# Kernel tuning notes

Hardware: AMD Instinct MI355X
Metric: run time of the kernel (lower is better)

Reference implementation:

```python
import jax, jax.numpy as jnp
import numpy as np

N = 50000   # nodes
E = 800000  # edges
NF = 16     # num_node_features
EF = 8      # num_edge_features
H = 4       # heads
C = 64      # out_channels per head
NC = 4      # num_classes


def setup_inputs() -> dict:
    key = jax.random.key(0)
    ks = jax.random.split(key, 32)
    w = lambda k, shape: (jax.random.normal(k, shape, jnp.float32) * 0.05)
    inp = {
        "x": jax.random.normal(ks[0], (N, NF), jnp.float32),
        "edge_index": jax.random.randint(ks[1], (2, E), 0, N, dtype=jnp.int32),
        "edge_attr": jax.random.normal(ks[2], (E, EF), jnp.float32),
        # fc00
        "w00": w(ks[3], (NF, 64)), "b00": jnp.zeros((64,), jnp.float32),
        # edge MLP
        "we1": w(ks[4], (EF, 64)), "be1": jnp.zeros((64,), jnp.float32),
        "we2": w(ks[5], (64, 64)), "be2": jnp.zeros((64,), jnp.float32),
        "we3": w(ks[6], (64, 64)), "be3": jnp.zeros((64,), jnp.float32),
        # TransformerConv projections (64 -> H*C = 256)
        "wq": w(ks[7], (64, H * C)), "bq": jnp.zeros((H * C,), jnp.float32),
        "wk": w(ks[8], (64, H * C)), "bk": jnp.zeros((H * C,), jnp.float32),
        "wv": w(ks[9], (64, H * C)), "bv": jnp.zeros((H * C,), jnp.float32),
        "wedge": w(ks[10], (64, H * C)), "bedge": jnp.zeros((H * C,), jnp.float32),
        "wskip": w(ks[11], (64, H * C)), "bskip": jnp.zeros((H * C,), jnp.float32),
        # LayerNorm(256)
        "ln_g": jnp.ones((H * C,), jnp.float32), "ln_b": jnp.zeros((H * C,), jnp.float32),
        # head
        "w1": w(ks[12], (H * C, 128)), "b1": jnp.zeros((128,), jnp.float32),
        "w2": w(ks[13], (128, NC)), "b2": jnp.zeros((NC,), jnp.float32),
    }
    return inp


def _forward(x, edge_attr, w00, b00, we1, be1, we2, be2, we3, be3,
             wq, bq, wk, bk, wv, bv, wedge, bedge, wskip, bskip,
             ln_g, ln_b, w1, b1, w2, b2, edge_index):
    relu = jax.nn.relu
    n = x.shape[0]
    # node embed (dropout = identity in eval)
    x1 = relu(x @ w00 + b00)                              # [N, 64]
    # edge MLP
    e = relu(edge_attr @ we1 + be1)
    e = relu(e @ we2 + be2)
    e = relu(e @ we3 + be3)                               # [E, 64]
    src, dst = edge_index[0], edge_index[1]
    # project nodes once, then gather per edge
    q = (x1 @ wq + bq).reshape(n, H, C)[dst]              # [E, H, C]
    k = (x1 @ wk + bk).reshape(n, H, C)[src]
    v = (x1 @ wv + bv).reshape(n, H, C)[src]
    eh = (e @ wedge + bedge).reshape(-1, H, C)            # [E, H, C]
    k = k + eh
    v = v + eh
    alpha = jnp.sum(q * k, axis=-1) / np.sqrt(C)          # [E, H]
    # segment softmax over incoming edges of each target node
    m = jax.ops.segment_max(alpha, dst, num_segments=n)   # [N, H]
    m = jnp.where(jnp.isfinite(m), m, 0.0)
    p = jnp.exp(alpha - m[dst])
    s = jax.ops.segment_sum(p, dst, num_segments=n)
    a = p / (s[dst] + 1e-16)                              # [E, H]
    out = jax.ops.segment_sum(v * a[:, :, None], dst, num_segments=n)
    out = out.reshape(n, H * C) + (x1 @ wskip + bskip)    # root skip (root_weight=True)
    # LayerNorm(256)
    mu = jnp.mean(out, axis=-1, keepdims=True)
    var = jnp.mean(jnp.square(out - mu), axis=-1, keepdims=True)
    out = (out - mu) * jax.lax.rsqrt(var + 1e-5) * ln_g + ln_b
    out = relu(out)
    h = relu(out @ w1 + b1)
    logits = h @ w2 + b2
    return jax.nn.log_softmax(logits, axis=1)


def reference(x, edge_index, edge_attr, w00, b00, we1, be1, we2, be2, we3, be3,
              wq, bq, wk, bk, wv, bv, wedge, bedge, wskip, bskip,
              ln_g, ln_b, w1, b1, w2, b2):
    return _forward(x, edge_attr, w00, b00, we1, be1, we2, be2, we3, be3,
                    wq, bq, wk, bk, wv, bv, wedge, bedge, wskip, bskip,
                    ln_g, ln_b, w1, b1, w2, b2, edge_index)
```

## Files before the change

kernel.cpp:

```cpp
#include <hip/hip_runtime.h>
#include <hip/hip_bf16.h>

typedef unsigned short u16;
typedef __attribute__((ext_vector_type(8))) short bf16x8;
typedef __attribute__((ext_vector_type(4))) float f32x4;

#define NN 50000
#define NE 800000
#define SCAN_NB ((NN + 255) / 256)

__device__ __forceinline__ float bf2f(u16 u) { return __uint_as_float(((unsigned)u) << 16); }
__device__ __forceinline__ u16 f2bf(float f) {
  unsigned u = __float_as_uint(f);
  return (u16)((u + 0x7FFFu + ((u >> 16) & 1u)) >> 16);
}

__global__ void k_zero(int* __restrict__ deg) {
  int i = blockIdx.x * 256 + threadIdx.x;
  if (i < NN) deg[i] = 0;
}

__global__ void k_hist(const int* __restrict__ ei, int* __restrict__ deg) {
  int i = blockIdx.x * 256 + threadIdx.x;
  if (i < NE) {
    int d = ei[NE + i];
    if (d >= 0 && d < NN) atomicAdd(&deg[d], 1);
  }
}

__global__ __launch_bounds__(256) void k_scan_a(const int* __restrict__ deg,
                                                int* __restrict__ bsum) {
  __shared__ int red[256];
  const int t = threadIdx.x;
  const int i = blockIdx.x * 256 + t;
  red[t] = (i < NN) ? deg[i] : 0;
  __syncthreads();
  #pragma unroll
  for (int s = 128; s > 0; s >>= 1) {
    if (t < s) red[t] += red[t + s];
    __syncthreads();
  }
  if (t == 0) bsum[blockIdx.x] = red[0];
}

__global__ __launch_bounds__(256) void k_scan_b(const int* __restrict__ bsum,
                                                int* __restrict__ boff,
                                                int* __restrict__ rowptr) {
  __shared__ int s[256];
  const int t = threadIdx.x;
  int v = (t < SCAN_NB) ? bsum[t] : 0;
  s[t] = v;
  __syncthreads();
  #pragma unroll
  for (int o = 1; o < 256; o <<= 1) {
    int u = (t >= o) ? s[t - o] : 0;
    __syncthreads();
    s[t] += u;
    __syncthreads();
  }
  if (t < SCAN_NB) boff[t] = s[t] - v;
  if (t == 255) rowptr[NN] = s[255];
}

__global__ __launch_bounds__(256) void k_scan_c(const int* __restrict__ deg,
                                                const int* __restrict__ boff,
                                                int* __restrict__ rowptr,
                                                int* __restrict__ cursor) {
  __shared__ int s[256];
  const int t = threadIdx.x;
  const int i = blockIdx.x * 256 + t;
  int v = (i < NN) ? deg[i] : 0;
  s[t] = v;
  __syncthreads();
  #pragma unroll
  for (int o = 1; o < 256; o <<= 1) {
    int u = (t >= o) ? s[t - o] : 0;
    __syncthreads();
    s[t] += u;
    __syncthreads();
  }
  if (i < NN) {
    int r = boff[blockIdx.x] + s[t] - v;
    rowptr[i] = r;
    cursor[i] = r;
  }
}

__global__ void k_scatter(const int* __restrict__ ei, int* __restrict__ cursor,
                          int* __restrict__ elist, int* __restrict__ slist) {
  int i = blockIdx.x * 256 + threadIdx.x;
  if (i < NE) {
    int d = ei[NE + i];
    if (d >= 0 && d < NN) {
      int pos = atomicAdd(&cursor[d], 1);
      if (pos >= 0 && pos < NE) {
        elist[pos] = i;
        int s = ei[i];
        slist[pos] = max(0, min(s, NN - 1));
      }
    }
  }
}

__global__ void k_prep(const float* __restrict__ wedge, const float* __restrict__ wk,
                       float* __restrict__ wT, float* __restrict__ wkT) {
  int i = blockIdx.x * 256 + threadIdx.x;
  if (i < 16384) {
    int c = i >> 6, j = i & 63;
    wT[i] = wedge[j * 256 + c];
  } else if (i < 32768) {
    int i2 = i - 16384;
    int c = i2 >> 6, j = i2 & 63;
    wkT[i2] = wk[j * 256 + c];
  }
}

__global__ void k_prep_w(const float* __restrict__ we1, const float* __restrict__ we2,
                         const float* __restrict__ we3,
                         u16* __restrict__ wB1t, u16* __restrict__ wB2t, u16* __restrict__ wB3t) {
  int i = blockIdx.x * 256 + threadIdx.x;
  if (i < 512) {
    int n = i >> 3, k = i & 7;
    wB1t[i] = f2bf(we1[k * 64 + n]);
  } else if (i < 512 + 4096) {
    int i2 = i - 512;
    int n = i2 >> 6, k = i2 & 63;
    wB2t[i2] = f2bf(we2[k * 64 + n]);
  } else if (i < 512 + 8192) {
    int i2 = i - 512 - 4096;
    int n = i2 >> 6, k = i2 & 63;
    wB3t[i2] = f2bf(we3[k * 64 + n]);
  }
}

__global__ void k_prep_b(const float* __restrict__ wedge, const float* __restrict__ wv,
                         const float* __restrict__ wskip, u16* __restrict__ Bt) {
  const int col = blockIdx.x;
  const int k = threadIdx.x;
  float v;
  if (k < 256) v = ((k >> 6) == (col >> 6)) ? wedge[(k & 63) * 256 + col] : 0.f;
  else if (k < 512) { int k2 = k - 256; v = ((k2 >> 6) == (col >> 6)) ? wv[(k2 & 63) * 256 + col] : 0.f; }
  else v = wskip[(k - 512) * 256 + col];
  Bt[col * 576 + k] = f2bf(v);
}

__global__ void k_prep_h(const float* __restrict__ w1, u16* __restrict__ Bt1) {
  const int col = blockIdx.x;
  const int k = threadIdx.x;
  Bt1[col * 256 + k] = f2bf(w1[k * 128 + col]);
}

__global__ __launch_bounds__(256) void k_node(
    const float* __restrict__ x, const float* __restrict__ w00, const float* __restrict__ b00,
    const float* __restrict__ wq, const float* __restrict__ bq,
    u16* __restrict__ x1g, u16* __restrict__ qg) {
  __shared__ float xs[128];
  __shared__ float x1s[8 * 65];
  const int t = threadIdx.x;
  const int n0 = blockIdx.x * 8;
  if (t < 128) xs[t] = x[n0 * 16 + t];
  __syncthreads();
  #pragma unroll
  for (int it = 0; it < 2; ++it) {
    int nb = it * 4 + (t >> 6);
    int col = t & 63;
    float v = b00[col];
    #pragma unroll
    for (int i = 0; i < 16; ++i) v += xs[nb * 16 + i] * w00[i * 64 + col];
    v = fmaxf(v, 0.f);
    x1s[nb * 65 + col] = v;
    x1g[(n0 + nb) * 64 + col] = f2bf(v);
  }
  __syncthreads();
  float aq[8];
  const float bqv = bq[t];
  #pragma unroll
  for (int nb = 0; nb < 8; ++nb) aq[nb] = bqv;
  for (int j = 0; j < 64; ++j) {
    float wqv = wq[j * 256 + t];
    #pragma unroll
    for (int nb = 0; nb < 8; ++nb) aq[nb] += x1s[nb * 65 + j] * wqv;
  }
  #pragma unroll
  for (int nb = 0; nb < 8; ++nb) qg[(n0 + nb) * 256 + t] = f2bf(aq[nb]);
}

__global__ __launch_bounds__(256) void k_gmat(const u16* __restrict__ qg,
                                              const float* __restrict__ wT,
                                              const float* __restrict__ wkT,
                                              u16* __restrict__ Gg, u16* __restrict__ Qkg) {
  __shared__ float qs[8 * 256];
  const int t = threadIdx.x;
  const int n0 = blockIdx.x * 8;
  #pragma unroll
  for (int i = 0; i < 8; ++i) qs[i * 256 + t] = bf2f(qg[(n0 + i) * 256 + t]);
  __syncthreads();
  const int h = t >> 6, j = t & 63;
  float accG[8] = {0, 0, 0, 0, 0, 0, 0, 0};
  float accK[8] = {0, 0, 0, 0, 0, 0, 0, 0};
  for (int c = 0; c < 64; ++c) {
    float wv = wT[(h * 64 + c) * 64 + j];
    float wk = wkT[(h * 64 + c) * 64 + j];
    #pragma unroll
    for (int nb = 0; nb < 8; ++nb) {
      float qv = qs[nb * 256 + h * 64 + c];
      accG[nb] += qv * wv;
      accK[nb] += qv * wk;
    }
  }
  #pragma unroll
  for (int nb = 0; nb < 8; ++nb) {
    Gg[(n0 + nb) * 256 + t] = f2bf(accG[nb]);
    Qkg[(n0 + nb) * 256 + t] = f2bf(accK[nb]);
  }
}

#define EPB 128
#define APAD 72
__global__ __launch_bounds__(256) void k_edge_mlp(
    const float* __restrict__ ea,
    const u16* __restrict__ wB1t, const u16* __restrict__ wB2t, const u16* __restrict__ wB3t,
    const float* __restrict__ be1, const float* __restrict__ be2, const float* __restrict__ be3,
    u16* __restrict__ e3g) {
  __shared__ u16 actA[EPB * APAD];
  __shared__ u16 actB[EPB * APAD];
  const int t = threadIdx.x;
  const int w = t >> 6, l = t & 63;
  const int quad = l >> 4, li = l & 15;
  const int e0 = blockIdx.x * EPB;
  const f32x4 zc = {0.f, 0.f, 0.f, 0.f};

  float b1c[4], b2c[4], b3c[4];
  #pragma unroll
  for (int nt = 0; nt < 4; ++nt) {
    b1c[nt] = be1[nt * 16 + li];
    b2c[nt] = be2[nt * 16 + li];
    b3c[nt] = be3[nt * 16 + li];
  }

  bf16x8 b1f[4];
  #pragma unroll
  for (int nt = 0; nt < 4; ++nt) {
    bf16x8 z = {};
    if (quad == 0) z = *(const bf16x8*)(wB1t + (nt * 16 + li) * 8);
    b1f[nt] = z;
  }
  #pragma unroll
  for (int mi = 0; mi < 2; ++mi) {
    const int mt = w * 2 + mi;
    bf16x8 af = {};
    if (quad == 0) {
      const float4* pa = (const float4*)(ea + (size_t)(e0 + mt * 16 + li) * 8);
      float4 p0 = pa[0], p1 = pa[1];
      af[0] = (short)f2bf(p0.x); af[1] = (short)f2bf(p0.y);
      af[2] = (short)f2bf(p0.z); af[3] = (short)f2bf(p0.w);
      af[4] = (short)f2bf(p1.x); af[5] = (short)f2bf(p1.y);
      af[6] = (short)f2bf(p1.z); af[7] = (short)f2bf(p1.w);
    }
    #pragma unroll
    for (int nt = 0; nt < 4; ++nt) {
      f32x4 d = __builtin_amdgcn_mfma_f32_16x16x32_bf16(af, b1f[nt], zc, 0, 0, 0);
      #pragma unroll
      for (int r = 0; r < 4; ++r)
        actA[(mt * 16 + quad * 4 + r) * APAD + nt * 16 + li] = f2bf(fmaxf(d[r] + b1c[nt], 0.f));
    }
  }
  __syncthreads();

  {
    bf16x8 bf[4][2];
    #pragma unroll
    for (int nt = 0; nt < 4; ++nt)
      #pragma unroll
      for (int kk = 0; kk < 2; ++kk)
        bf[nt][kk] = *(const bf16x8*)(wB2t + (nt * 16 + li) * 64 + kk * 32 + quad * 8);
    #pragma unroll
    for (int mi = 0; mi < 2; ++mi) {
      const int mt = w * 2 + mi;
      bf16x8 a0 = *(const bf16x8*)(actA + (mt * 16 + li) * APAD + quad * 8);
      bf16x8 a1 = *(const bf16x8*)(actA + (mt * 16 + li) * APAD + 32 + quad * 8);
      #pragma unroll
      for (int nt = 0; nt < 4; ++nt) {
        f32x4 d = __builtin_amdgcn_mfma_f32_16x16x32_bf16(a0, bf[nt][0], zc, 0, 0, 0);
        d = __builtin_amdgcn_mfma_f32_16x16x32_bf16(a1, bf[nt][1], d, 0, 0, 0);
        #pragma unroll
        for (int r = 0; r < 4; ++r)
          actB[(mt * 16 + quad * 4 + r) * APAD + nt * 16 + li] = f2bf(fmaxf(d[r] + b2c[nt], 0.f));
      }
    }
  }
  __syncthreads();

  {
    bf16x8 bf[4][2];
    #pragma unroll
    for (int nt = 0; nt < 4; ++nt)
      #pragma unroll
      for (int kk = 0; kk < 2; ++kk)
        bf[nt][kk] = *(const bf16x8*)(wB3t + (nt * 16 + li) * 64 + kk * 32 + quad * 8);
    #pragma unroll
    for (int mi = 0; mi < 2; ++mi) {
      const int mt = w * 2 + mi;
      bf16x8 a0 = *(const bf16x8*)(actB + (mt * 16 + li) * APAD + quad * 8);
      bf16x8 a1 = *(const bf16x8*)(actB + (mt * 16 + li) * APAD + 32 + quad * 8);
      #pragma unroll
      for (int nt = 0; nt < 4; ++nt) {
        f32x4 d = __builtin_amdgcn_mfma_f32_16x16x32_bf16(a0, bf[nt][0], zc, 0, 0, 0);
        d = __builtin_amdgcn_mfma_f32_16x16x32_bf16(a1, bf[nt][1], d, 0, 0, 0);
        #pragma unroll
        for (int r = 0; r < 4; ++r)
          actA[(mt * 16 + quad * 4 + r) * APAD + nt * 16 + li] = f2bf(fmaxf(d[r] + b3c[nt], 0.f));
      }
    }
  }
  __syncthreads();

  #pragma unroll
  for (int it = 0; it < 4; ++it) {
    int flat = it * 2048 + t * 8;
    int el = flat >> 6, c = flat & 63;
    uint4 v = *(const uint4*)(actA + el * APAD + c);
    *(uint4*)(e3g + (size_t)(e0 + el) * 64 + c) = v;
  }
}

__global__ __launch_bounds__(256) void k_attn(
    const int* __restrict__ rowptr, const int* __restrict__ elist, const int* __restrict__ slist,
    u16* qo, const u16* __restrict__ x1g, u16* gz, const u16* __restrict__ Qkg,
    const u16* __restrict__ e3g,
    const float* __restrict__ bk, const float* __restrict__ bedge,
    float* __restrict__ bfac) {
  const int t = threadIdx.x;
  const int w = t >> 6;
  const int l = t & 63;
  const int grp = l >> 4;
  const int li = l & 15;
  const int chb = grp * 64 + li * 4;
  const int n = blockIdx.x * 4 + w;
  int base = rowptr[n];
  int end  = rowptr[n + 1];
  base = max(0, min(base, NE));
  end  = max(base, min(end, NE));
  if (l == 0) bfac[n] = (end > base) ? 1.f : 0.f;

  float Qkf[4], Gf[4];
  {
    ushort4 kv = *(const ushort4*)(Qkg + (size_t)n * 256 + chb);
    Qkf[0] = bf2f(kv.x); Qkf[1] = bf2f(kv.y); Qkf[2] = bf2f(kv.z); Qkf[3] = bf2f(kv.w);
    ushort4 gv = *(const ushort4*)(gz + (size_t)n * 256 + chb);
    Gf[0] = bf2f(gv.x); Gf[1] = bf2f(gv.y); Gf[2] = bf2f(gv.z); Gf[3] = bf2f(gv.w);
  }
  float bqe;
  {
    ushort4 qv = *(const ushort4*)(qo + (size_t)n * 256 + chb);
    float4 bkv = *(const float4*)(bk + chb);
    float4 bev = *(const float4*)(bedge + chb);
    bqe = bf2f(qv.x) * (bkv.x + bev.x) + bf2f(qv.y) * (bkv.y + bev.y)
        + bf2f(qv.z) * (bkv.z + bev.z) + bf2f(qv.w) * (bkv.w + bev.w);
    #pragma unroll
    for (int mk = 1; mk < 16; mk <<= 1) bqe += __shfl_xor(bqe, mk);
  }

  float s_run = 0.f;
  float y[4] = {0, 0, 0, 0}, zz[4] = {0, 0, 0, 0};
  int d = base;
  for (; d + 1 < end; d += 2) {
    int eid0 = elist[d],     src0 = slist[d];
    int eid1 = elist[d + 1], src1 = slist[d + 1];
    eid0 = max(0, min(eid0, NE - 1)); eid1 = max(0, min(eid1, NE - 1));
    src0 = max(0, min(src0, NN - 1)); src1 = max(0, min(src1, NN - 1));
    ushort4 x0 = *(const ushort4*)(x1g + (size_t)src0 * 64 + li * 4);
    ushort4 e0 = *(const ushort4*)(e3g + (size_t)eid0 * 64 + li * 4);
    ushort4 x1v = *(const ushort4*)(x1g + (size_t)src1 * 64 + li * 4);
    ushort4 e1 = *(const ushort4*)(e3g + (size_t)eid1 * 64 + li * 4);
    float xf00 = bf2f(x0.x), xf01 = bf2f(x0.y), xf02 = bf2f(x0.z), xf03 = bf2f(x0.w);
    float ef00 = bf2f(e0.x), ef01 = bf2f(e0.y), ef02 = bf2f(e0.z), ef03 = bf2f(e0.w);
    float xf10 = bf2f(x1v.x), xf11 = bf2f(x1v.y), xf12 = bf2f(x1v.z), xf13 = bf2f(x1v.w);
    float ef10 = bf2f(e1.x), ef11 = bf2f(e1.y), ef12 = bf2f(e1.z), ef13 = bf2f(e1.w);
    float p0 = Qkf[0]*xf00 + Qkf[1]*xf01 + Qkf[2]*xf02 + Qkf[3]*xf03
             + Gf[0]*ef00 + Gf[1]*ef01 + Gf[2]*ef02 + Gf[3]*ef03;
    float p1 = Qkf[0]*xf10 + Qkf[1]*xf11 + Qkf[2]*xf12 + Qkf[3]*xf13
             + Gf[0]*ef10 + Gf[1]*ef11 + Gf[2]*ef12 + Gf[3]*ef13;
    #pragma unroll
    for (int mk = 1; mk < 16; mk <<= 1) { p0 += __shfl_xor(p0, mk); p1 += __shfl_xor(p1, mk); }
    float w0 = __expf(fminf((p0 + bqe) * 0.125f, 60.f));
    float w1 = __expf(fminf((p1 + bqe) * 0.125f, 60.f));
    s_run += w0 + w1;
    y[0] += w0*xf00 + w1*xf10; y[1] += w0*xf01 + w1*xf11;
    y[2] += w0*xf02 + w1*xf12; y[3] += w0*xf03 + w1*xf13;
    zz[0] += w0*ef00 + w1*ef10; zz[1] += w0*ef01 + w1*ef11;
    zz[2] += w0*ef02 + w1*ef12; zz[3] += w0*ef03 + w1*ef13;
  }
  if (d < end) {
    int eid0 = elist[d], src0 = slist[d];
    eid0 = max(0, min(eid0, NE - 1));
    src0 = max(0, min(src0, NN - 1));
    ushort4 x0 = *(const ushort4*)(x1g + (size_t)src0 * 64 + li * 4);
    ushort4 e0 = *(const ushort4*)(e3g + (size_t)eid0 * 64 + li * 4);
    float xf00 = bf2f(x0.x), xf01 = bf2f(x0.y), xf02 = bf2f(x0.z), xf03 = bf2f(x0.w);
    float ef00 = bf2f(e0.x), ef01 = bf2f(e0.y), ef02 = bf2f(e0.z), ef03 = bf2f(e0.w);
    float p0 = Qkf[0]*xf00 + Qkf[1]*xf01 + Qkf[2]*xf02 + Qkf[3]*xf03
             + Gf[0]*ef00 + Gf[1]*ef01 + Gf[2]*ef02 + Gf[3]*ef03;
    #pragma unroll
    for (int mk = 1; mk < 16; mk <<= 1) p0 += __shfl_xor(p0, mk);
    float w0 = __expf(fminf((p0 + bqe) * 0.125f, 60.f));
    s_run += w0;
    y[0] += w0*xf00; y[1] += w0*xf01; y[2] += w0*xf02; y[3] += w0*xf03;
    zz[0] += w0*ef00; zz[1] += w0*ef01; zz[2] += w0*ef02; zz[3] += w0*ef03;
  }
  const float inv_s = 1.0f / (s_run + 1e-16f);
  ushort4 ynv, znv;
  ynv.x = f2bf(y[0] * inv_s); ynv.y = f2bf(y[1] * inv_s);
  ynv.z = f2bf(y[2] * inv_s); ynv.w = f2bf(y[3] * inv_s);
  znv.x = f2bf(zz[0] * inv_s); znv.y = f2bf(zz[1] * inv_s);
  znv.z = f2bf(zz[2] * inv_s); znv.w = f2bf(zz[3] * inv_s);
  *(ushort4*)(qo + (size_t)n * 256 + chb) = ynv;
  *(ushort4*)(gz + (size_t)n * 256 + chb) = znv;
}

#define PM 64
#define PK 576
#define PAPAD 584
__global__ __launch_bounds__(256) void k_post(
    const u16* __restrict__ zng, const u16* __restrict__ yng, const u16* __restrict__ x1g,
    const u16* __restrict__ Bt, const float* __restrict__ bfac,
    const float* __restrict__ bedge, const float* __restrict__ bv, const float* __restrict__ bskip,
    const float* __restrict__ lng, const float* __restrict__ lnb,
    u16* __restrict__ postg) {
  __shared__ u16 As[PM * PAPAD];
  __shared__ float ps1[PM * 4];
  __shared__ float ps2[PM * 4];
  const int t = threadIdx.x;
  const int w = t >> 6, l = t & 63;
  const int quad = l >> 4, li = l & 15;
  const int n0 = blockIdx.x * PM;

  for (int q = t; q < 2048; q += 256) {
    int row = q >> 5, off = (q & 31) * 8;
    uint4 vz = make_uint4(0, 0, 0, 0), vy = make_uint4(0, 0, 0, 0);
    if (n0 + row < NN) {
      vz = *(const uint4*)(zng + (size_t)(n0 + row) * 256 + off);
      vy = *(const uint4*)(yng + (size_t)(n0 + row) * 256 + off);
    }
    *(uint4*)(As + row * PAPAD + off) = vz;
    *(uint4*)(As + row * PAPAD + 256 + off) = vy;
  }
  for (int q = t; q < 512; q += 256) {
    int row = q >> 3, off = (q & 7) * 8;
    uint4 v = make_uint4(0, 0, 0, 0);
    if (n0 + row < NN) v = *(const uint4*)(x1g + (size_t)(n0 + row) * 64 + off);
    *(uint4*)(As + row * PAPAD + 512 + off) = v;
  }
  __syncthreads();

  f32x4 acc[4][4];
  #pragma unroll
  for (int mt = 0; mt < 4; ++mt)
    #pragma unroll
    for (int nt = 0; nt < 4; ++nt) acc[mt][nt] = (f32x4){0.f, 0.f, 0.f, 0.f};

  const int colbase = w * 64;
  #pragma unroll
  for (int s = 0; s < 18; ++s) {
    bf16x8 bf[4];
    #pragma unroll
    for (int nt = 0; nt < 4; ++nt)
      bf[nt] = *(const bf16x8*)(Bt + (size_t)(colbase + nt * 16 + li) * PK + s * 32 + quad * 8);
    #pragma unroll
    for (int mt = 0; mt < 4; ++mt) {
      bf16x8 af = *(const bf16x8*)(As + (mt * 16 + li) * PAPAD + s * 32 + quad * 8);
      #pragma unroll
      for (int nt = 0; nt < 4; ++nt)
        acc[mt][nt] = __builtin_amdgcn_mfma_f32_16x16x32_bf16(af, bf[nt], acc[mt][nt], 0, 0, 0);
    }
  }

  float beb[4], bs4[4], g4[4], lb4[4];
  #pragma unroll
  for (int nt = 0; nt < 4; ++nt) {
    int col = colbase + nt * 16 + li;
    beb[nt] = bedge[col] + bv[col];
    bs4[nt] = bskip[col]; g4[nt] = lng[col]; lb4[nt] = lnb[col];
  }
  #pragma unroll
  for (int mt = 0; mt < 4; ++mt) {
    #pragma unroll
    for (int r = 0; r < 4; ++r) {
      int node = n0 + mt * 16 + quad * 4 + r;
      float hasE = bfac[min(node, NN - 1)];
      #pragma unroll
      for (int nt = 0; nt < 4; ++nt)
        acc[mt][nt][r] += hasE * beb[nt] + bs4[nt];
    }
  }
  #pragma unroll
  for (int mt = 0; mt < 4; ++mt)
    #pragma unroll
    for (int r = 0; r < 4; ++r) {
      float s = acc[mt][0][r] + acc[mt][1][r] + acc[mt][2][r] + acc[mt][3][r];
      #pragma unroll
      for (int mk = 1; mk < 16; mk <<= 1) s += __shfl_xor(s, mk);
      if (li == 0) ps1[(mt * 16 + quad * 4 + r) * 4 + w] = s;
    }
  __syncthreads();
  float mu[4][4];
  #pragma unroll
  for (int mt = 0; mt < 4; ++mt)
    #pragma unroll
    for (int r = 0; r < 4; ++r) {
      float4 p = *(const float4*)(ps1 + (mt * 16 + quad * 4 + r) * 4);
      mu[mt][r] = (p.x + p.y + p.z + p.w) * (1.0f / 256.0f);
    }
  #pragma unroll
  for (int mt = 0; mt < 4; ++mt)
    #pragma unroll
    for (int r = 0; r < 4; ++r) {
      float m = mu[mt][r];
      float s = 0.f;
      #pragma unroll
      for (int nt = 0; nt < 4; ++nt) { float dd = acc[mt][nt][r] - m; s += dd * dd; }
      #pragma unroll
      for (int mk = 1; mk < 16; mk <<= 1) s += __shfl_xor(s, mk);
      if (li == 0) ps2[(mt * 16 + quad * 4 + r) * 4 + w] = s;
    }
  __syncthreads();
  #pragma unroll
  for (int mt = 0; mt < 4; ++mt)
    #pragma unroll
    for (int r = 0; r < 4; ++r) {
      float4 p = *(const float4*)(ps2 + (mt * 16 + quad * 4 + r) * 4);
      float rstd = rsqrtf((p.x + p.y + p.z + p.w) * (1.0f / 256.0f) + 1e-5f);
      int node = n0 + mt * 16 + quad * 4 + r;
      if (node < NN) {
        float m = mu[mt][r];
        #pragma unroll
        for (int nt = 0; nt < 4; ++nt) {
          int col = colbase + nt * 16 + li;
          postg[(size_t)node * 256 + col] =
              f2bf(fmaxf((acc[mt][nt][r] - m) * rstd * g4[nt] + lb4[nt], 0.f));
        }
      }
    }
}

#define HAPAD 264
#define H1PAD 136
__global__ __launch_bounds__(256) void k_head(
    const u16* __restrict__ postg, const u16* __restrict__ Bt1,
    const float* __restrict__ b1, const float* __restrict__ w2, const float* __restrict__ b2,
    float* __restrict__ outg) {
  __shared__ u16 As[64 * HAPAD];
  __shared__ u16 h1s[64 * H1PAD];
  const int t = threadIdx.x;
  const int w = t >> 6, l = t & 63;
  const int quad = l >> 4, li = l & 15;
  const int n0 = blockIdx.x * 64;

  for (int q = t; q < 2048; q += 256) {
    int row = q >> 5, off = (q & 31) * 8;
    uint4 v = make_uint4(0, 0, 0, 0);
    if (n0 + row < NN) v = *(const uint4*)(postg + (size_t)(n0 + row) * 256 + off);
    *(uint4*)(As + row * HAPAD + off) = v;
  }
  __syncthreads();

  f32x4 acc[4][2];
  #pragma unroll
  for (int mt = 0; mt < 4; ++mt)
    #pragma unroll
    for (int nt = 0; nt < 2; ++nt) acc[mt][nt] = (f32x4){0.f, 0.f, 0.f, 0.f};
  const int colbase = w * 32;
  #pragma unroll
  for (int s = 0; s < 8; ++s) {
    bf16x8 bf[2];
    #pragma unroll
    for (int nt = 0; nt < 2; ++nt)
      bf[nt] = *(const bf16x8*)(Bt1 + (size_t)(colbase + nt * 16 + li) * 256 + s * 32 + quad * 8);
    #pragma unroll
    for (int mt = 0; mt < 4; ++mt) {
      bf16x8 af = *(const bf16x8*)(As + (mt * 16 + li) * HAPAD + s * 32 + quad * 8);
      #pragma unroll
      for (int nt = 0; nt < 2; ++nt)
        acc[mt][nt] = __builtin_amdgcn_mfma_f32_16x16x32_bf16(af, bf[nt], acc[mt][nt], 0, 0, 0);
    }
  }
  float b1c[2];
  #pragma unroll
  for (int nt = 0; nt < 2; ++nt) b1c[nt] = b1[colbase + nt * 16 + li];
  #pragma unroll
  for (int mt = 0; mt < 4; ++mt)
    #pragma unroll
    for (int nt = 0; nt < 2; ++nt)
      #pragma unroll
      for (int r = 0; r < 4; ++r)
        h1s[(mt * 16 + quad * 4 + r) * H1PAD + colbase + nt * 16 + li] =
            f2bf(fmaxf(acc[mt][nt][r] + b1c[nt], 0.f));
  __syncthreads();

  const int node = t >> 2, c = t & 3;
  float lg = b2[c];
  const u16* hrow = h1s + node * H1PAD;
  #pragma unroll 4
  for (int j = 0; j < 128; ++j) lg += bf2f(hrow[j]) * w2[j * 4 + c];
  float mx = lg;
  #pragma unroll
  for (int mk = 1; mk < 4; mk <<= 1) mx = fmaxf(mx, __shfl_xor(mx, mk));
  float ex = __expf(lg - mx);
  float se = ex;
  #pragma unroll
  for (int mk = 1; mk < 4; mk <<= 1) se += __shfl_xor(se, mk);
  float res = lg - (mx + __logf(se));
  if (n0 + node < NN) outg[(size_t)(n0 + node) * 4 + c] = res;
}

extern "C" void kernel_launch(void* const* d_in, const int* in_sizes, int n_in,
                              void* d_out, int out_size, void* d_ws, size_t ws_size,
                              hipStream_t stream) {
  const float* x     = (const float*)d_in[0];
  const int*   ei    = (const int*)d_in[1];
  const float* ea    = (const float*)d_in[2];
  const float* w00   = (const float*)d_in[3];
  const float* b00   = (const float*)d_in[4];
  const float* we1   = (const float*)d_in[5];
  const float* be1   = (const float*)d_in[6];
  const float* we2   = (const float*)d_in[7];
  const float* be2   = (const float*)d_in[8];
  const float* we3   = (const float*)d_in[9];
  const float* be3   = (const float*)d_in[10];
  const float* wq    = (const float*)d_in[11];
  const float* bq    = (const float*)d_in[12];
  const float* wk    = (const float*)d_in[13];
  const float* bk    = (const float*)d_in[14];
  const float* wv    = (const float*)d_in[15];
  const float* bv    = (const float*)d_in[16];
  const float* wedge = (const float*)d_in[17];
  const float* bedge = (const float*)d_in[18];
  const float* wskip = (const float*)d_in[19];
  const float* bskip = (const float*)d_in[20];
  const float* lng   = (const float*)d_in[21];
  const float* lnb   = (const float*)d_in[22];
  const float* w1    = (const float*)d_in[23];
  const float* b1    = (const float*)d_in[24];
  const float* w2    = (const float*)d_in[25];
  const float* b2    = (const float*)d_in[26];
  float* outg = (float*)d_out;

  size_t off = 0;
  char* wsb = (char*)d_ws;
  auto carve = [&](size_t bytes) -> char* {
    char* r = wsb + off;
    off += (bytes + 255) & ~(size_t)255;
    return r;
  };
  u16* qg     = (u16*)carve((size_t)NN * 256 * 2);
  u16* Gg     = (u16*)carve((size_t)NN * 256 * 2);
  u16* Qkg    = (u16*)carve((size_t)NN * 256 * 2);
  u16* x1g    = (u16*)carve((size_t)NN * 64 * 2);
  u16* e3g    = (u16*)carve((size_t)NE * 64 * 2);
  int* deg    = (int*)carve((size_t)NN * 4);
  int* rowptr = (int*)carve((size_t)(NN + 1) * 4);
  int* cursor = (int*)carve((size_t)NN * 4);
  int* elist  = (int*)carve((size_t)NE * 4);
  int* slist  = (int*)carve((size_t)NE * 4);
  float* bfac = (float*)carve((size_t)NN * 4);
  int* bsum   = (int*)carve((size_t)SCAN_NB * 4);
  int* boff   = (int*)carve((size_t)SCAN_NB * 4);
  float* wT   = (float*)carve(16384 * 4);
  float* wkT  = (float*)carve(16384 * 4);
  u16* wB1t   = (u16*)carve(512 * 2);
  u16* wB2t   = (u16*)carve(4096 * 2);
  u16* wB3t   = (u16*)carve(4096 * 2);
  u16* Bt     = (u16*)carve((size_t)256 * 576 * 2);
  u16* Bt1    = (u16*)carve((size_t)128 * 256 * 2);
  u16* postg  = e3g;
  if (off > ws_size) return;

  k_prep<<<128, 256, 0, stream>>>(wedge, wk, wT, wkT);
  k_prep_w<<<34, 256, 0, stream>>>(we1, we2, we3, wB1t, wB2t, wB3t);
  k_prep_b<<<256, 576, 0, stream>>>(wedge, wv, wskip, Bt);
  k_prep_h<<<128, 256, 0, stream>>>(w1, Bt1);
  k_zero<<<SCAN_NB, 256, 0, stream>>>(deg);
  k_hist<<<NE / 256, 256, 0, stream>>>(ei, deg);
  k_scan_a<<<SCAN_NB, 256, 0, stream>>>(deg, bsum);
  k_scan_b<<<1, 256, 0, stream>>>(bsum, boff, rowptr);
  k_scan_c<<<SCAN_NB, 256, 0, stream>>>(deg, boff, rowptr, cursor);
  k_scatter<<<NE / 256, 256, 0, stream>>>(ei, cursor, elist, slist);
  k_node<<<NN / 8, 256, 0, stream>>>(x, w00, b00, wq, bq, x1g, qg);
  k_gmat<<<NN / 8, 256, 0, stream>>>(qg, wT, wkT, Gg, Qkg);
  k_edge_mlp<<<NE / EPB, 256, 0, stream>>>(ea, wB1t, wB2t, wB3t, be1, be2, be3, e3g);
  k_attn<<<NN / 4, 256, 0, stream>>>(rowptr, elist, slist, qg, x1g, Gg, Qkg, e3g, bk, bedge, bfac);
  k_post<<<(NN + PM - 1) / PM, 256, 0, stream>>>(Gg, qg, x1g, Bt, bfac, bedge, bv, bskip,
                                                 lng, lnb, postg);
  k_head<<<(NN + 63) / 64, 256, 0, stream>>>(postg, Bt1, b1, w2, b2, outg);
}
```

Baseline: 565.4 us.

## Fuse node and G-matrix kernels, write edge features in CSR order, drop bias term

Merges k_node and k_gmat so q stays in shared memory instead of being written to and reread from global as bf16. The scatter now records each edge's CSR position, and the edge MLP writes its output directly in destination-sorted order, so the attention loop reads edge features contiguously with no elist indirection. The constant per-node q·(bk+bedge) term is removed from the logits because it cancels in the softmax. The cost is a scattered write in the edge MLP, and the softmax loses the max-subtraction shift that term provided, relying on the existing clamp at 60.

```diff
diff --git a/kernel.cpp b/kernel.cpp
--- a/kernel.cpp
+++ b/kernel.cpp
@@ -87,14 +87,14 @@
 }
 
 __global__ void k_scatter(const int* __restrict__ ei, int* __restrict__ cursor,
-                          int* __restrict__ elist, int* __restrict__ slist) {
+                          int* __restrict__ slist, int* __restrict__ e2p) {
   int i = blockIdx.x * 256 + threadIdx.x;
   if (i < NE) {
     int d = ei[NE + i];
     if (d >= 0 && d < NN) {
       int pos = atomicAdd(&cursor[d], 1);
       if (pos >= 0 && pos < NE) {
-        elist[pos] = i;
+        e2p[i] = pos;
         int s = ei[i];
         slist[pos] = max(0, min(s, NN - 1));
       }
@@ -150,12 +150,14 @@
   Bt1[col * 256 + k] = f2bf(w1[k * 128 + col]);
 }
 
-__global__ __launch_bounds__(256) void k_node(
+__global__ __launch_bounds__(256) void k_ng(
     const float* __restrict__ x, const float* __restrict__ w00, const float* __restrict__ b00,
     const float* __restrict__ wq, const float* __restrict__ bq,
-    u16* __restrict__ x1g, u16* __restrict__ qg) {
+    const float* __restrict__ wT, const float* __restrict__ wkT,
+    u16* __restrict__ x1g, u16* __restrict__ Gg, u16* __restrict__ Qkg) {
   __shared__ float xs[128];
   __shared__ float x1s[8 * 65];
+  __shared__ float qs[8 * 256];
   const int t = threadIdx.x;
   const int n0 = blockIdx.x * 8;
   if (t < 128) xs[t] = x[n0 * 16 + t];
@@ -172,28 +174,19 @@
     x1g[(n0 + nb) * 64 + col] = f2bf(v);
   }
   __syncthreads();
-  float aq[8];
-  const float bqv = bq[t];
-  #pragma unroll
-  for (int nb = 0; nb < 8; ++nb) aq[nb] = bqv;
-  for (int j = 0; j < 64; ++j) {
-    float wqv = wq[j * 256 + t];
-    #pragma unroll
-    for (int nb = 0; nb < 8; ++nb) aq[nb] += x1s[nb * 65 + j] * wqv;
-  }
-  #pragma unroll
-  for (int nb = 0; nb < 8; ++nb) qg[(n0 + nb) * 256 + t] = f2bf(aq[nb]);
-}
-
-__global__ __launch_bounds__(256) void k_gmat(const u16* __restrict__ qg,
-                                              const float* __restrict__ wT,
-                                              const float* __restrict__ wkT,
-                                              u16* __restrict__ Gg, u16* __restrict__ Qkg) {
-  __shared__ float qs[8 * 256];
-  const int t = threadIdx.x;
-  const int n0 = blockIdx.x * 8;
-  #pragma unroll
-  for (int i = 0; i < 8; ++i) qs[i * 256 + t] = bf2f(qg[(n0 + i) * 256 + t]);
+  {
+    float aq[8];
+    const float bqv = bq[t];
+    #pragma unroll
+    for (int nb = 0; nb < 8; ++nb) aq[nb] = bqv;
+    for (int j = 0; j < 64; ++j) {
+      float wqv = wq[j * 256 + t];
+      #pragma unroll
+      for (int nb = 0; nb < 8; ++nb) aq[nb] += x1s[nb * 65 + j] * wqv;
+    }
+    #pragma unroll
+    for (int nb = 0; nb < 8; ++nb) qs[nb * 256 + t] = aq[nb];
+  }
   __syncthreads();
   const int h = t >> 6, j = t & 63;
   float accG[8] = {0, 0, 0, 0, 0, 0, 0, 0};
@@ -221,7 +214,7 @@
     const float* __restrict__ ea,
     const u16* __restrict__ wB1t, const u16* __restrict__ wB2t, const u16* __restrict__ wB3t,
     const float* __restrict__ be1, const float* __restrict__ be2, const float* __restrict__ be3,
-    u16* __restrict__ e3g) {
+    const int* __restrict__ e2p, u16* __restrict__ e3g) {
   __shared__ u16 actA[EPB * APAD];
   __shared__ u16 actB[EPB * APAD];
   const int t = threadIdx.x;
@@ -319,17 +312,17 @@
   for (int it = 0; it < 4; ++it) {
     int flat = it * 2048 + t * 8;
     int el = flat >> 6, c = flat & 63;
+    int pos = e2p[e0 + el];
+    pos = ((unsigned)pos <= (unsigned)(NE - 1)) ? pos : NE;
     uint4 v = *(const uint4*)(actA + el * APAD + c);
-    *(uint4*)(e3g + (size_t)(e0 + el) * 64 + c) = v;
+    *(uint4*)(e3g + (size_t)pos * 64 + c) = v;
   }
 }
 
 __global__ __launch_bounds__(256) void k_attn(
-    const int* __restrict__ rowptr, const int* __restrict__ elist, const int* __restrict__ slist,
-    u16* qo, const u16* __restrict__ x1g, u16* gz, const u16* __restrict__ Qkg,
-    const u16* __restrict__ e3g,
-    const float* __restrict__ bk, const float* __restrict__ bedge,
-    float* __restrict__ bfac) {
+    const int* __restrict__ rowptr, const int* __restrict__ slist,
+    u16* yo, const u16* __restrict__ x1g, u16* gz, const u16* __restrict__ Qkg,
+    const u16* __restrict__ e3g, float* __restrict__ bfac) {
   const int t = threadIdx.x;
   const int w = t >> 6;
   const int l = t & 63;
@@ -350,29 +343,17 @@
     ushort4 gv = *(const ushort4*)(gz + (size_t)n * 256 + chb);
     Gf[0] = bf2f(gv.x); Gf[1] = bf2f(gv.y); Gf[2] = bf2f(gv.z); Gf[3] = bf2f(gv.w);
   }
-  float bqe;
-  {
-    ushort4 qv = *(const ushort4*)(qo + (size_t)n * 256 + chb);
-    float4 bkv = *(const float4*)(bk + chb);
-    float4 bev = *(const float4*)(bedge + chb);
-    bqe = bf2f(qv.x) * (bkv.x + bev.x) + bf2f(qv.y) * (bkv.y + bev.y)
-        + bf2f(qv.z) * (bkv.z + bev.z) + bf2f(qv.w) * (bkv.w + bev.w);
-    #pragma unroll
-    for (int mk = 1; mk < 16; mk <<= 1) bqe += __shfl_xor(bqe, mk);
-  }
 
   float s_run = 0.f;
   float y[4] = {0, 0, 0, 0}, zz[4] = {0, 0, 0, 0};
   int d = base;
   for (; d + 1 < end; d += 2) {
-    int eid0 = elist[d],     src0 = slist[d];
-    int eid1 = elist[d + 1], src1 = slist[d + 1];
-    eid0 = max(0, min(eid0, NE - 1)); eid1 = max(0, min(eid1, NE - 1));
+    int src0 = slist[d], src1 = slist[d + 1];
     src0 = max(0, min(src0, NN - 1)); src1 = max(0, min(src1, NN - 1));
     ushort4 x0 = *(const ushort4*)(x1g + (size_t)src0 * 64 + li * 4);
-    ushort4 e0 = *(const ushort4*)(e3g + (size_t)eid0 * 64 + li * 4);
+    ushort4 e0 = *(const ushort4*)(e3g + (size_t)d * 64 + li * 4);
     ushort4 x1v = *(const ushort4*)(x1g + (size_t)src1 * 64 + li * 4);
-    ushort4 e1 = *(const ushort4*)(e3g + (size_t)eid1 * 64 + li * 4);
+    ushort4 e1 = *(const ushort4*)(e3g + (size_t)(d + 1) * 64 + li * 4);
     float xf00 = bf2f(x0.x), xf01 = bf2f(x0.y), xf02 = bf2f(x0.z), xf03 = bf2f(x0.w);
     float ef00 = bf2f(e0.x), ef01 = bf2f(e0.y), ef02 = bf2f(e0.z), ef03 = bf2f(e0.w);
     float xf10 = bf2f(x1v.x), xf11 = bf2f(x1v.y), xf12 = bf2f(x1v.z), xf13 = bf2f(x1v.w);
@@ -383,8 +364,8 @@
              + Gf[0]*ef10 + Gf[1]*ef11 + Gf[2]*ef12 + Gf[3]*ef13;
     #pragma unroll
     for (int mk = 1; mk < 16; mk <<= 1) { p0 += __shfl_xor(p0, mk); p1 += __shfl_xor(p1, mk); }
-    float w0 = __expf(fminf((p0 + bqe) * 0.125f, 60.f));
-    float w1 = __expf(fminf((p1 + bqe) * 0.125f, 60.f));
+    float w0 = __expf(fminf(p0 * 0.125f, 60.f));
+    float w1 = __expf(fminf(p1 * 0.125f, 60.f));
     s_run += w0 + w1;
     y[0] += w0*xf00 + w1*xf10; y[1] += w0*xf01 + w1*xf11;
     y[2] += w0*xf02 + w1*xf12; y[3] += w0*xf03 + w1*xf13;
@@ -392,18 +373,17 @@
     zz[2] += w0*ef02 + w1*ef12; zz[3] += w0*ef03 + w1*ef13;
   }
   if (d < end) {
-    int eid0 = elist[d], src0 = slist[d];
-    eid0 = max(0, min(eid0, NE - 1));
+    int src0 = slist[d];
     src0 = max(0, min(src0, NN - 1));
     ushort4 x0 = *(const ushort4*)(x1g + (size_t)src0 * 64 + li * 4);
-    ushort4 e0 = *(const ushort4*)(e3g + (size_t)eid0 * 64 + li * 4);
+    ushort4 e0 = *(const ushort4*)(e3g + (size_t)d * 64 + li * 4);
     float xf00 = bf2f(x0.x), xf01 = bf2f(x0.y), xf02 = bf2f(x0.z), xf03 = bf2f(x0.w);
     float ef00 = bf2f(e0.x), ef01 = bf2f(e0.y), ef02 = bf2f(e0.z), ef03 = bf2f(e0.w);
     float p0 = Qkf[0]*xf00 + Qkf[1]*xf01 + Qkf[2]*xf02 + Qkf[3]*xf03
              + Gf[0]*ef00 + Gf[1]*ef01 + Gf[2]*ef02 + Gf[3]*ef03;
     #pragma unroll
     for (int mk = 1; mk < 16; mk <<= 1) p0 += __shfl_xor(p0, mk);
-    float w0 = __expf(fminf((p0 + bqe) * 0.125f, 60.f));
+    float w0 = __expf(fminf(p0 * 0.125f, 60.f));
     s_run += w0;
     y[0] += w0*xf00; y[1] += w0*xf01; y[2] += w0*xf02; y[3] += w0*xf03;
     zz[0] += w0*ef00; zz[1] += w0*ef01; zz[2] += w0*ef02; zz[3] += w0*ef03;
@@ -414,7 +394,7 @@
   ynv.z = f2bf(y[2] * inv_s); ynv.w = f2bf(y[3] * inv_s);
   znv.x = f2bf(zz[0] * inv_s); znv.y = f2bf(zz[1] * inv_s);
   znv.z = f2bf(zz[2] * inv_s); znv.w = f2bf(zz[3] * inv_s);
-  *(ushort4*)(qo + (size_t)n * 256 + chb) = ynv;
+  *(ushort4*)(yo + (size_t)n * 256 + chb) = ynv;
   *(ushort4*)(gz + (size_t)n * 256 + chb) = znv;
 }
 
@@ -644,6 +624,7 @@
   const float* w2    = (const float*)d_in[25];
   const float* b2    = (const float*)d_in[26];
   float* outg = (float*)d_out;
+  (void)bk;
 
   size_t off = 0;
   char* wsb = (char*)d_ws;
@@ -652,16 +633,16 @@
     off += (bytes + 255) & ~(size_t)255;
     return r;
   };
-  u16* qg     = (u16*)carve((size_t)NN * 256 * 2);
+  u16* yg     = (u16*)carve((size_t)NN * 256 * 2);
   u16* Gg     = (u16*)carve((size_t)NN * 256 * 2);
   u16* Qkg    = (u16*)carve((size_t)NN * 256 * 2);
   u16* x1g    = (u16*)carve((size_t)NN * 64 * 2);
-  u16* e3g    = (u16*)carve((size_t)NE * 64 * 2);
+  u16* e3g    = (u16*)carve((size_t)(NE + 1) * 64 * 2);
   int* deg    = (int*)carve((size_t)NN * 4);
   int* rowptr = (int*)carve((size_t)(NN + 1) * 4);
   int* cursor = (int*)carve((size_t)NN * 4);
-  int* elist  = (int*)carve((size_t)NE * 4);
   int* slist  = (int*)carve((size_t)NE * 4);
+  int* e2p    = (int*)carve((size_t)NE * 4);
   float* bfac = (float*)carve((size_t)NN * 4);
   int* bsum   = (int*)carve((size_t)SCAN_NB * 4);
   int* boff   = (int*)carve((size_t)SCAN_NB * 4);
@@ -684,12 +665,11 @@
   k_scan_a<<<SCAN_NB, 256, 0, stream>>>(deg, bsum);
   k_scan_b<<<1, 256, 0, stream>>>(bsum, boff, rowptr);
   k_scan_c<<<SCAN_NB, 256, 0, stream>>>(deg, boff, rowptr, cursor);
-  k_scatter<<<NE / 256, 256, 0, stream>>>(ei, cursor, elist, slist);
-  k_node<<<NN / 8, 256, 0, stream>>>(x, w00, b00, wq, bq, x1g, qg);
-  k_gmat<<<NN / 8, 256, 0, stream>>>(qg, wT, wkT, Gg, Qkg);
-  k_edge_mlp<<<NE / EPB, 256, 0, stream>>>(ea, wB1t, wB2t, wB3t, be1, be2, be3, e3g);
-  k_attn<<<NN / 4, 256, 0, stream>>>(rowptr, elist, slist, qg, x1g, Gg, Qkg, e3g, bk, bedge, bfac);
-  k_post<<<(NN + PM - 1) / PM, 256, 0, stream>>>(Gg, qg, x1g, Bt, bfac, bedge, bv, bskip,
+  k_scatter<<<NE / 256, 256, 0, stream>>>(ei, cursor, slist, e2p);
+  k_ng<<<NN / 8, 256, 0, stream>>>(x, w00, b00, wq, bq, wT, wkT, x1g, Gg, Qkg);
+  k_edge_mlp<<<NE / EPB, 256, 0, stream>>>(ea, wB1t, wB2t, wB3t, be1, be2, be3, e2p, e3g);
+  k_attn<<<NN / 4, 256, 0, stream>>>(rowptr, slist, yg, x1g, Gg, Qkg, e3g, bfac);
+  k_post<<<(NN + PM - 1) / PM, 256, 0, stream>>>(Gg, yg, x1g, Bt, bfac, bedge, bv, bskip,
                                                  lng, lnb, postg);
   k_head<<<(NN + 63) / 64, 256, 0, stream>>>(postg, Bt1, b1, w2, b2, outg);
 }
```

Result: faster. 550.8 us (-2.6%).
